# Performance work log

Hardware: AMD Instinct MI355X
Metric: run time of the kernel (lower is better)

Reference implementation:

```python
import jax, jax.numpy as jnp
import numpy as np

N = 100000      # nodes
K = 16          # neighbors per node
C_IN = 16
C1 = 64
C2 = 128
C_OUT = 40


def setup_inputs() -> dict:
    key = jax.random.key(0)
    ks = jax.random.split(key, 12)
    x = jax.random.normal(ks[0], (N, C_IN), dtype=jnp.float32)
    # kNN-style edge list: row = arange(N) repeated K times, col = neighbor ids
    row = jnp.repeat(jnp.arange(N, dtype=jnp.int32), K)
    col = jax.random.randint(ks[1], (N * K,), 0, N, dtype=jnp.int32)
    edge_index = jnp.stack([row, col], axis=0)  # [2, E]
    s = 0.02
    params = {
        'W1': jax.random.normal(ks[2], (2 * C_IN, C1), jnp.float32) * s,
        'b1': jnp.zeros((C1,), jnp.float32),
        'W2': jax.random.normal(ks[3], (C1, C1), jnp.float32) * s,
        'b2': jnp.zeros((C1,), jnp.float32),
        'W3': jax.random.normal(ks[4], (2 * C1, C2), jnp.float32) * s,
        'b3': jnp.zeros((C2,), jnp.float32),
        'W4': jax.random.normal(ks[5], (C2, C2), jnp.float32) * s,
        'b4': jnp.zeros((C2,), jnp.float32),
        'W5': jax.random.normal(ks[6], (C2, C2), jnp.float32) * s,
        'b5': jnp.zeros((C2,), jnp.float32),
        'W6': jax.random.normal(ks[7], (C2, C_OUT), jnp.float32) * s,
        'b6': jnp.zeros((C_OUT,), jnp.float32),
    }
    return {'x': x, 'edge_index': edge_index, **params}


def _edge_conv(x, row, col, Wa, ba, Wb, bb):
    # gather + diff + concat: [E, 2*C]
    xr = x[row]
    e = jnp.concatenate([xr, x[col] - xr], axis=-1)
    h = jax.nn.relu(e @ Wa + ba)
    return jax.nn.relu(h @ Wb + bb)


def reference(x, edge_index, W1, b1, W2, b2, W3, b3, W4, b4, W5, b5, W6, b6):
    row, col = edge_index[0], edge_index[1]
    h1 = _edge_conv(x, row, col, W1, b1, W2, b2)      # [E, 64]
    # as in the source, conv2 indexes the edge-feature tensor with node ids
    h2 = _edge_conv(h1, row, col, W3, b3, W4, b4)     # [E, 128]
    # max over the K neighbors of each node (edges grouped by row node)
    g = h2.reshape(N, K, C2).max(axis=1)              # [N, 128]
    out = jax.nn.relu(g @ W5 + b5) @ W6 + b6          # [N, out]
    return out
```

## Files before the change

kernel.cpp:

```cpp
#include <hip/hip_runtime.h>


#define NN 100000
#define KNB 16
#define EE (NN * KNB)

#define W2F 0
#define W3F 8
#define W4F 40
#define W5F 72
#define W6F 104
#define NFRAG 116

typedef float floatx4 __attribute__((ext_vector_type(4)));
typedef __bf16 bf16x8 __attribute__((ext_vector_type(8)));

static __device__ __forceinline__ unsigned f2bf_rne_u(float f) {
    unsigned u = __float_as_uint(f);
    return (u + 0x7FFFu + ((u >> 16) & 1u)) >> 16;
}
static __device__ __forceinline__ float bfu2f(unsigned h) {
    return __uint_as_float(h << 16);
}

static __device__ __forceinline__ void split_pack2(float a, float b,
                                                   unsigned& hp, unsigned& lp) {
    unsigned ua = __float_as_uint(a), ub = __float_as_uint(b);
    hp = __builtin_amdgcn_perm(ub, ua, 0x07060302u);
    float ra = a - __uint_as_float(ua & 0xFFFF0000u);
    float rb = b - __uint_as_float(ub & 0xFFFF0000u);
    unsigned la = __float_as_uint(ra), lb = __float_as_uint(rb);
    la = la + 0x7FFFu + ((la >> 16) & 1u);
    lb = lb + 0x7FFFu + ((lb >> 16) & 1u);
    lp = __builtin_amdgcn_perm(lb, la, 0x07060302u);
}

static __device__ __forceinline__ void split8(float4 f0, float4 f1,
                                              bf16x8& ah, bf16x8& al) {
    unsigned hd[4], ld[4];
    split_pack2(f0.x, f0.y, hd[0], ld[0]);
    split_pack2(f0.z, f0.w, hd[1], ld[1]);
    split_pack2(f1.x, f1.y, hd[2], ld[2]);
    split_pack2(f1.z, f1.w, hd[3], ld[3]);
    uint4 H = {hd[0], hd[1], hd[2], hd[3]};
    uint4 L = {ld[0], ld[1], ld[2], ld[3]};
    ah = __builtin_bit_cast(bf16x8, H);
    al = __builtin_bit_cast(bf16x8, L);
}

__global__ __launch_bounds__(256) void kw_kernel(
    const float* __restrict__ W2, const float* __restrict__ W3,
    const float* __restrict__ W4, const float* __restrict__ W5,
    const float* __restrict__ W6,
    unsigned short* __restrict__ WH, unsigned short* __restrict__ WL)
{
    int d = blockIdx.x * 256 + threadIdx.x;
    if (d >= NFRAG * 64) return;
    int f = d >> 6, l = d & 63, c = l & 15, q = l >> 4;
    float v[8];
    if (f < W3F) {
        int fx = f - W2F, kc = fx >> 2, nt = fx & 3;
        int k0 = kc * 32 + q * 8, n = nt * 16 + c;
#pragma unroll
        for (int j = 0; j < 8; ++j) v[j] = W2[(k0 + j) * 64 + n];
    } else if (f < W4F) {
        int fx = f - W3F, kc = fx >> 4, nt = fx & 15;
        int k0 = kc * 32 + q * 8, n = nt * 16 + c;
#pragma unroll
        for (int j = 0; j < 8; ++j) {
            int k = k0 + j;
            v[j] = (n < 128) ? (W3[k * 128 + n] - W3[(64 + k) * 128 + n])
                             : W3[(64 + k) * 128 + (n - 128)];
        }
    } else if (f < W5F) {
        int fx = f - W4F, kc = fx >> 3, nt = fx & 7;
        int k0 = kc * 32 + q * 8, n = nt * 16 + c;
#pragma unroll
        for (int j = 0; j < 8; ++j) v[j] = W4[(k0 + j) * 128 + n];
    } else if (f < W6F) {
        int fx = f - W5F, kc = fx >> 3, nt = fx & 7;
        int k0 = kc * 32 + q * 8, n = nt * 16 + c;
#pragma unroll
        for (int j = 0; j < 8; ++j) v[j] = W5[(k0 + j) * 128 + n];
    } else {
        int fx = f - W6F, kc = fx / 3, nt = fx % 3;
        int k0 = kc * 32 + q * 8, n = nt * 16 + c;
#pragma unroll
        for (int j = 0; j < 8; ++j)
            v[j] = (n < 40) ? W6[(k0 + j) * 40 + n] : 0.0f;
    }
    unsigned hs[8], ls[8];
#pragma unroll
    for (int j = 0; j < 8; ++j) {
        unsigned h = f2bf_rne_u(v[j]);
        float r = v[j] - bfu2f(h);
        hs[j] = h;
        ls[j] = f2bf_rne_u(r);
    }
    uint4 H, L;
    H.x = hs[0] | (hs[1] << 16); H.y = hs[2] | (hs[3] << 16);
    H.z = hs[4] | (hs[5] << 16); H.w = hs[6] | (hs[7] << 16);
    L.x = ls[0] | (ls[1] << 16); L.y = ls[2] | (ls[3] << 16);
    L.z = ls[4] | (ls[5] << 16); L.w = ls[6] | (ls[7] << 16);
    *(uint4*)(WH + (size_t)d * 8) = H;
    *(uint4*)(WL + (size_t)d * 8) = L;
}

__global__ __launch_bounds__(256) void k1_kernel(
    const float* __restrict__ x, const float* __restrict__ W1,
    const float* __restrict__ b1, float* __restrict__ A1, float* __restrict__ B1)
{
    int gid = blockIdx.x * 256 + threadIdx.x;
    int n = gid >> 6;
    int j = gid & 63;
    const float* xr = x + n * 16;
    float acc_a = b1[j];
    float acc_b = 0.0f;
#pragma unroll
    for (int k = 0; k < 16; ++k) {
        float xv = xr[k];
        float wt = W1[k * 64 + j];
        float wb = W1[(16 + k) * 64 + j];
        acc_a = fmaf(xv, wt - wb, acc_a);
        acc_b = fmaf(xv, wb, acc_b);
    }
    A1[n * 64 + j] = acc_a;
    B1[n * 64 + j] = acc_b;
}

__global__ __launch_bounds__(256) void k2_kernel(
    const int* __restrict__ col,
    const float* __restrict__ A1, const float* __restrict__ B1,
    const unsigned short* __restrict__ WH, const unsigned short* __restrict__ WL,
    const float* __restrict__ b2, const float* __restrict__ b3,
    float* __restrict__ A3, float* __restrict__ B3)
{
    __shared__ __align__(16) float tF[8 * 512];
    __shared__ __align__(16) float hF[8 * 512];
    const int t = threadIdx.x;
    const int i0 = blockIdx.x * 64;

    {
        const int row = t & 63, part = t >> 6;
        int i = i0 + row;
        int nn = i >> 4;
        int ci = col[i];
        const float* ar = A1 + (size_t)nn * 64 + part * 16;
        const float* br = B1 + (size_t)ci * 64 + part * 16;
        int mt = row >> 4, m = row & 15, kc = part >> 1;
        float* base = tF + (mt * 2 + kc) * 512 + m * 8;
#pragma unroll
        for (int h = 0; h < 2; ++h) {
            int qq = (part & 1) * 2 + h;
            float4 a0 = *(const float4*)(ar + h * 8);
            float4 b0 = *(const float4*)(br + h * 8);
            float4 a1 = *(const float4*)(ar + h * 8 + 4);
            float4 b1v = *(const float4*)(br + h * 8 + 4);
            float4 r0, r1;
            r0.x = fmaxf(a0.x + b0.x, 0.0f); r0.y = fmaxf(a0.y + b0.y, 0.0f);
            r0.z = fmaxf(a0.z + b0.z, 0.0f); r0.w = fmaxf(a0.w + b0.w, 0.0f);
            r1.x = fmaxf(a1.x + b1v.x, 0.0f); r1.y = fmaxf(a1.y + b1v.y, 0.0f);
            r1.z = fmaxf(a1.z + b1v.z, 0.0f); r1.w = fmaxf(a1.w + b1v.w, 0.0f);
            *(float4*)(base + qq * 128) = r0;
            *(float4*)(base + qq * 128 + 4) = r1;
        }
    }
    __syncthreads();

    const int w = __builtin_amdgcn_readfirstlane(t >> 6);
    const int lane = t & 63;

    floatx4 acc1[4];
#pragma unroll
    for (int nt = 0; nt < 4; ++nt) acc1[nt] = (floatx4){0.f, 0.f, 0.f, 0.f};
#pragma unroll
    for (int kc = 0; kc < 2; ++kc) {
        const float* ap = tF + (w * 2 + kc) * 512 + lane * 8;
        bf16x8 ah, al;
        split8(*(const float4*)ap, *(const float4*)(ap + 4), ah, al);
#pragma unroll
        for (int nt = 0; nt < 4; ++nt) {
            size_t fb = (size_t)(W2F + kc * 4 + nt) * 512 + lane * 8;
            bf16x8 bh = __builtin_bit_cast(bf16x8, *(const uint4*)(WH + fb));
            bf16x8 bl = __builtin_bit_cast(bf16x8, *(const uint4*)(WL + fb));
            acc1[nt] = __builtin_amdgcn_mfma_f32_16x16x32_bf16(ah, bh, acc1[nt], 0, 0, 0);
            acc1[nt] = __builtin_amdgcn_mfma_f32_16x16x32_bf16(ah, bl, acc1[nt], 0, 0, 0);
            acc1[nt] = __builtin_amdgcn_mfma_f32_16x16x32_bf16(al, bh, acc1[nt], 0, 0, 0);
        }
    }
    {
        const int qq = lane >> 4, cc = lane & 15;
#pragma unroll
        for (int nt = 0; nt < 4; ++nt) {
            float bv = b2[nt * 16 + cc];
            int colIdx = nt * 16 + cc;
            int kc2 = colIdx >> 5, q2 = (colIdx >> 3) & 3, jj = cc & 7;
            float* dst = hF + (w * 2 + kc2) * 512 + q2 * 128 + jj;
#pragma unroll
            for (int r = 0; r < 4; ++r)
                dst[(qq * 4 + r) * 8] = fmaxf(acc1[nt][r] + bv, 0.0f);
        }
    }
    floatx4 acc2[16];
#pragma unroll
    for (int nt = 0; nt < 16; ++nt) acc2[nt] = (floatx4){0.f, 0.f, 0.f, 0.f};
#pragma unroll
    for (int kc = 0; kc < 2; ++kc) {
        const float* ap = hF + (w * 2 + kc) * 512 + lane * 8;
        bf16x8 ah, al;
        split8(*(const float4*)ap, *(const float4*)(ap + 4), ah, al);
#pragma unroll
        for (int nt = 0; nt < 16; ++nt) {
            size_t fb = (size_t)(W3F + kc * 16 + nt) * 512 + lane * 8;
            bf16x8 bh = __builtin_bit_cast(bf16x8, *(const uint4*)(WH + fb));
            bf16x8 bl = __builtin_bit_cast(bf16x8, *(const uint4*)(WL + fb));
            acc2[nt] = __builtin_amdgcn_mfma_f32_16x16x32_bf16(ah, bh, acc2[nt], 0, 0, 0);
            acc2[nt] = __builtin_amdgcn_mfma_f32_16x16x32_bf16(ah, bl, acc2[nt], 0, 0, 0);
            acc2[nt] = __builtin_amdgcn_mfma_f32_16x16x32_bf16(al, bh, acc2[nt], 0, 0, 0);
        }
    }
    {
        const int qq = lane >> 4, cc = lane & 15;
#pragma unroll
        for (int nt = 0; nt < 16; ++nt) {
            int n = nt * 16 + cc;
            float bv = (n < 128) ? b3[n] : 0.0f;
#pragma unroll
            for (int r = 0; r < 4; ++r) {
                int i = i0 + w * 16 + qq * 4 + r;
                if (i < NN) {
                    float vv = acc2[nt][r];
                    if (n < 128) A3[(size_t)i * 128 + n] = vv + bv;
                    else         B3[(size_t)i * 128 + (n - 128)] = vv;
                }
            }
        }
    }
}

__global__ __launch_bounds__(256) void k3_kernel(
    const int* __restrict__ col,
    const float* __restrict__ A3, const float* __restrict__ B3,
    const unsigned short* __restrict__ WH, const unsigned short* __restrict__ WL,
    const float* __restrict__ b4, float* __restrict__ g)
{
    __shared__ __align__(16) unsigned short aHi[8192];
    __shared__ __align__(16) unsigned short aLo[8192];
    const int t = threadIdx.x;
    const int node0 = blockIdx.x * 4;
    const int e0 = node0 * KNB;
    const int row = t & 63;
    const int kcm = t >> 6;

    {
        const int c = col[e0 + row];
        const int mt = row >> 4, m = row & 15;
        const float* brow = B3 + (size_t)c * 128 + kcm * 32;
        const float* arow = A3 + (size_t)(node0 + mt) * 128 + kcm * 32;
        const int base = (mt * 4 + kcm) * 512 + m * 8;
#pragma unroll
        for (int q = 0; q < 4; ++q) {
            float4 b0 = *(const float4*)(brow + q * 8);
            float4 b1 = *(const float4*)(brow + q * 8 + 4);
            float4 a0 = *(const float4*)(arow + q * 8);
            float4 a1 = *(const float4*)(arow + q * 8 + 4);
            float v0 = fmaxf(a0.x + b0.x, 0.0f), v1 = fmaxf(a0.y + b0.y, 0.0f);
            float v2 = fmaxf(a0.z + b0.z, 0.0f), v3 = fmaxf(a0.w + b0.w, 0.0f);
            float v4 = fmaxf(a1.x + b1.x, 0.0f), v5 = fmaxf(a1.y + b1.y, 0.0f);
            float v6 = fmaxf(a1.z + b1.z, 0.0f), v7 = fmaxf(a1.w + b1.w, 0.0f);
            uint4 H, L;
            split_pack2(v0, v1, H.x, L.x);
            split_pack2(v2, v3, H.y, L.y);
            split_pack2(v4, v5, H.z, L.z);
            split_pack2(v6, v7, H.w, L.w);
            *(uint4*)(aHi + base + q * 128) = H;
            *(uint4*)(aLo + base + q * 128) = L;
        }
    }
    __syncthreads();

    const int wv = t >> 6;
    const int lane = t & 63;
    const int ntb = wv * 2;
    floatx4 acc[4][2];
#pragma unroll
    for (int mt = 0; mt < 4; ++mt)
#pragma unroll
        for (int ntl = 0; ntl < 2; ++ntl)
            acc[mt][ntl] = (floatx4){0.0f, 0.0f, 0.0f, 0.0f};

    for (int kc = 0; kc < 4; ++kc) {
        bf16x8 bh[2], bl[2];
#pragma unroll
        for (int ntl = 0; ntl < 2; ++ntl) {
            int nt = ntb + ntl;
            bh[ntl] = __builtin_bit_cast(bf16x8,
                *(const uint4*)(WH + (size_t)((kc * 8 + nt) * 64 + lane) * 8));
            bl[ntl] = __builtin_bit_cast(bf16x8,
                *(const uint4*)(WL + (size_t)((kc * 8 + nt) * 64 + lane) * 8));
        }
        bf16x8 ah[4], al[4];
#pragma unroll
        for (int mt = 0; mt < 4; ++mt) {
            ah[mt] = __builtin_bit_cast(bf16x8,
                *(const uint4*)(aHi + (mt * 4 + kc) * 512 + lane * 8));
            al[mt] = __builtin_bit_cast(bf16x8,
                *(const uint4*)(aLo + (mt * 4 + kc) * 512 + lane * 8));
        }
#pragma unroll
        for (int mt = 0; mt < 4; ++mt)
#pragma unroll
            for (int ntl = 0; ntl < 2; ++ntl) {
                acc[mt][ntl] = __builtin_amdgcn_mfma_f32_16x16x32_bf16(
                    ah[mt], bh[ntl], acc[mt][ntl], 0, 0, 0);
                acc[mt][ntl] = __builtin_amdgcn_mfma_f32_16x16x32_bf16(
                    ah[mt], bl[ntl], acc[mt][ntl], 0, 0, 0);
                acc[mt][ntl] = __builtin_amdgcn_mfma_f32_16x16x32_bf16(
                    al[mt], bh[ntl], acc[mt][ntl], 0, 0, 0);
            }
    }

#pragma unroll
    for (int mt = 0; mt < 4; ++mt)
#pragma unroll
        for (int ntl = 0; ntl < 2; ++ntl) {
            floatx4 a = acc[mt][ntl];
            float mm = fmaxf(fmaxf(a[0], a[1]), fmaxf(a[2], a[3]));
            mm = fmaxf(mm, __shfl_xor(mm, 16));
            mm = fmaxf(mm, __shfl_xor(mm, 32));
            if (lane < 16) {
                int ccol = (ntb + ntl) * 16 + lane;
                g[(size_t)(node0 + mt) * 128 + ccol] =
                    fmaxf(mm + b4[ccol], 0.0f);
            }
        }
}

__global__ __launch_bounds__(256) void k4_kernel(
    const float* __restrict__ g,
    const unsigned short* __restrict__ WH, const unsigned short* __restrict__ WL,
    const float* __restrict__ b5, const float* __restrict__ b6,
    float* __restrict__ out)
{
    __shared__ __align__(16) float gF[16 * 512];
    const int t = threadIdx.x;
    const int n0 = blockIdx.x * 64;

    {
        const int row = t & 63, part = t >> 6;
        int gn = n0 + row; if (gn >= NN) gn = NN - 1;
        const float* gr = g + (size_t)gn * 128 + part * 32;
        int mt = row >> 4, m = row & 15;
        float* base = gF + (mt * 4 + part) * 512 + m * 8;
#pragma unroll
        for (int qq = 0; qq < 4; ++qq) {
            *(float4*)(base + qq * 128)     = *(const float4*)(gr + qq * 8);
            *(float4*)(base + qq * 128 + 4) = *(const float4*)(gr + qq * 8 + 4);
        }
    }
    __syncthreads();

    const int w = __builtin_amdgcn_readfirstlane(t >> 6);
    const int lane = t & 63;

    floatx4 acc1[8];
#pragma unroll
    for (int nt = 0; nt < 8; ++nt) acc1[nt] = (floatx4){0.f, 0.f, 0.f, 0.f};
#pragma unroll
    for (int kc = 0; kc < 4; ++kc) {
        const float* ap = gF + (w * 4 + kc) * 512 + lane * 8;
        bf16x8 ah, al;
        split8(*(const float4*)ap, *(const float4*)(ap + 4), ah, al);
#pragma unroll
        for (int nt = 0; nt < 8; ++nt) {
            size_t fb = (size_t)(W5F + kc * 8 + nt) * 512 + lane * 8;
            bf16x8 bh = __builtin_bit_cast(bf16x8, *(const uint4*)(WH + fb));
            bf16x8 bl = __builtin_bit_cast(bf16x8, *(const uint4*)(WL + fb));
            acc1[nt] = __builtin_amdgcn_mfma_f32_16x16x32_bf16(ah, bh, acc1[nt], 0, 0, 0);
            acc1[nt] = __builtin_amdgcn_mfma_f32_16x16x32_bf16(ah, bl, acc1[nt], 0, 0, 0);
            acc1[nt] = __builtin_amdgcn_mfma_f32_16x16x32_bf16(al, bh, acc1[nt], 0, 0, 0);
        }
    }
    {
        const int qq = lane >> 4, cc = lane & 15;
#pragma unroll
        for (int nt = 0; nt < 8; ++nt) {
            float bv = b5[nt * 16 + cc];
            int colIdx = nt * 16 + cc;
            int kc2 = colIdx >> 5, q2 = (colIdx >> 3) & 3, jj = cc & 7;
            float* dst = gF + (w * 4 + kc2) * 512 + q2 * 128 + jj;
#pragma unroll
            for (int r = 0; r < 4; ++r)
                dst[(qq * 4 + r) * 8] = fmaxf(acc1[nt][r] + bv, 0.0f);
        }
    }
    floatx4 acc2[3];
#pragma unroll
    for (int nt = 0; nt < 3; ++nt) acc2[nt] = (floatx4){0.f, 0.f, 0.f, 0.f};
#pragma unroll
    for (int kc = 0; kc < 4; ++kc) {
        const float* ap = gF + (w * 4 + kc) * 512 + lane * 8;
        bf16x8 ah, al;
        split8(*(const float4*)ap, *(const float4*)(ap + 4), ah, al);
#pragma unroll
        for (int nt = 0; nt < 3; ++nt) {
            size_t fb = (size_t)(W6F + kc * 3 + nt) * 512 + lane * 8;
            bf16x8 bh = __builtin_bit_cast(bf16x8, *(const uint4*)(WH + fb));
            bf16x8 bl = __builtin_bit_cast(bf16x8, *(const uint4*)(WL + fb));
            acc2[nt] = __builtin_amdgcn_mfma_f32_16x16x32_bf16(ah, bh, acc2[nt], 0, 0, 0);
            acc2[nt] = __builtin_amdgcn_mfma_f32_16x16x32_bf16(ah, bl, acc2[nt], 0, 0, 0);
            acc2[nt] = __builtin_amdgcn_mfma_f32_16x16x32_bf16(al, bh, acc2[nt], 0, 0, 0);
        }
    }
    {
        const int qq = lane >> 4, cc = lane & 15;
#pragma unroll
        for (int nt = 0; nt < 3; ++nt) {
            int n = nt * 16 + cc;
            if (n < 40) {
                float bv = b6[n];
#pragma unroll
                for (int r = 0; r < 4; ++r) {
                    int i = n0 + w * 16 + qq * 4 + r;
                    if (i < NN)
                        out[(size_t)i * 40 + n] = acc2[nt][r] + bv;
                }
            }
        }
    }
}

extern "C" void kernel_launch(void* const* d_in, const int* in_sizes, int n_in,
                              void* d_out, int out_size, void* d_ws, size_t ws_size,
                              hipStream_t stream)
{
    const float* x  = (const float*)d_in[0];
    const int* ei   = (const int*)d_in[1];
    const int* col  = ei + EE;
    const float* W1 = (const float*)d_in[2];
    const float* b1 = (const float*)d_in[3];
    const float* W2 = (const float*)d_in[4];
    const float* b2 = (const float*)d_in[5];
    const float* W3 = (const float*)d_in[6];
    const float* b3 = (const float*)d_in[7];
    const float* W4 = (const float*)d_in[8];
    const float* b4 = (const float*)d_in[9];
    const float* W5 = (const float*)d_in[10];
    const float* b5 = (const float*)d_in[11];
    const float* W6 = (const float*)d_in[12];
    const float* b6 = (const float*)d_in[13];
    float* out = (float*)d_out;

    float* A1 = (float*)d_ws;
    float* B1 = A1 + (size_t)NN * 64;
    float* A3 = B1 + (size_t)NN * 64;
    float* B3 = A3 + (size_t)NN * 128;
    unsigned short* WH = (unsigned short*)(B3 + (size_t)NN * 128);
    unsigned short* WL = WH + NFRAG * 512;
    float* g  = A1;

    kw_kernel<<<(NFRAG * 64 + 255) / 256, 256, 0, stream>>>(W2, W3, W4, W5, W6, WH, WL);
    k1_kernel<<<NN * 64 / 256, 256, 0, stream>>>(x, W1, b1, A1, B1);
    k2_kernel<<<(NN + 63) / 64, 256, 0, stream>>>(col, A1, B1, WH, WL, b2, b3, A3, B3);
    k3_kernel<<<NN / 4, 256, 0, stream>>>(col, A3, B3,
                                          WH + (size_t)W4F * 512, WL + (size_t)W4F * 512,
                                          b4, g);
    k4_kernel<<<(NN + 63) / 64, 256, 0, stream>>>(g, WH, WL, b5, b6, out);
}
```

Baseline: 482.5 us.

## Build k3 MFMA A-fragments in registers, two nodes per wave

The k3 kernel no longer stages the gathered, ReLU'd, bf16-split edge features in shared memory behind a __syncthreads. Each lane now loads its A3/B3 slices directly into the MFMA A-fragment layout, and each wave owns two nodes across all 128 output columns. Blocks cover 8 nodes instead of 4, which halves the grid and lets each weight fragment load feed two nodes. This removes LDS traffic and the block barrier, but raises register pressure (16 accumulators plus 16 A fragments) and each lane now reads 32-byte pieces with strided access.

New measurement: 572.7 us. +18.7%, slower.

```diff
diff --git a/kernel.cpp b/kernel.cpp
--- a/kernel.cpp
+++ b/kernel.cpp
@@ -244,26 +244,25 @@
     const unsigned short* __restrict__ WH, const unsigned short* __restrict__ WL,
     const float* __restrict__ b4, float* __restrict__ g)
 {
-    __shared__ __align__(16) unsigned short aHi[8192];
-    __shared__ __align__(16) unsigned short aLo[8192];
     const int t = threadIdx.x;
-    const int node0 = blockIdx.x * 4;
-    const int e0 = node0 * KNB;
-    const int row = t & 63;
-    const int kcm = t >> 6;
-
-    {
-        const int c = col[e0 + row];
-        const int mt = row >> 4, m = row & 15;
-        const float* brow = B3 + (size_t)c * 128 + kcm * 32;
-        const float* arow = A3 + (size_t)(node0 + mt) * 128 + kcm * 32;
-        const int base = (mt * 4 + kcm) * 512 + m * 8;
-#pragma unroll
-        for (int q = 0; q < 4; ++q) {
-            float4 b0 = *(const float4*)(brow + q * 8);
-            float4 b1 = *(const float4*)(brow + q * 8 + 4);
-            float4 a0 = *(const float4*)(arow + q * 8);
-            float4 a1 = *(const float4*)(arow + q * 8 + 4);
+    const int w = t >> 6;
+    const int lane = t & 63;
+    const int m = lane & 15, q = lane >> 4;
+    const int nodeBase = blockIdx.x * 8 + w * 2;
+
+    bf16x8 aH[2][4], aL[2][4];
+#pragma unroll
+    for (int ng = 0; ng < 2; ++ng) {
+        const int node = nodeBase + ng;
+        const int c = col[node * KNB + m];
+        const float* br = B3 + (size_t)c * 128 + q * 8;
+        const float* ar = A3 + (size_t)node * 128 + q * 8;
+#pragma unroll
+        for (int kc = 0; kc < 4; ++kc) {
+            float4 b0 = *(const float4*)(br + kc * 32);
+            float4 b1 = *(const float4*)(br + kc * 32 + 4);
+            float4 a0 = *(const float4*)(ar + kc * 32);
+            float4 a1 = *(const float4*)(ar + kc * 32 + 4);
             float v0 = fmaxf(a0.x + b0.x, 0.0f), v1 = fmaxf(a0.y + b0.y, 0.0f);
             float v2 = fmaxf(a0.z + b0.z, 0.0f), v3 = fmaxf(a0.w + b0.w, 0.0f);
             float v4 = fmaxf(a1.x + b1.x, 0.0f), v5 = fmaxf(a1.y + b1.y, 0.0f);
@@ -273,67 +272,52 @@
             split_pack2(v2, v3, H.y, L.y);
             split_pack2(v4, v5, H.z, L.z);
             split_pack2(v6, v7, H.w, L.w);
-            *(uint4*)(aHi + base + q * 128) = H;
-            *(uint4*)(aLo + base + q * 128) = L;
-        }
-    }
-    __syncthreads();
-
-    const int wv = t >> 6;
-    const int lane = t & 63;
-    const int ntb = wv * 2;
-    floatx4 acc[4][2];
-#pragma unroll
-    for (int mt = 0; mt < 4; ++mt)
-#pragma unroll
-        for (int ntl = 0; ntl < 2; ++ntl)
-            acc[mt][ntl] = (floatx4){0.0f, 0.0f, 0.0f, 0.0f};
-
+            aH[ng][kc] = __builtin_bit_cast(bf16x8, H);
+            aL[ng][kc] = __builtin_bit_cast(bf16x8, L);
+        }
+    }
+
+    floatx4 acc[2][8];
+#pragma unroll
+    for (int ng = 0; ng < 2; ++ng)
+#pragma unroll
+        for (int nt = 0; nt < 8; ++nt)
+            acc[ng][nt] = (floatx4){0.0f, 0.0f, 0.0f, 0.0f};
+
+#pragma unroll
     for (int kc = 0; kc < 4; ++kc) {
-        bf16x8 bh[2], bl[2];
-#pragma unroll
-        for (int ntl = 0; ntl < 2; ++ntl) {
-            int nt = ntb + ntl;
-            bh[ntl] = __builtin_bit_cast(bf16x8,
-                *(const uint4*)(WH + (size_t)((kc * 8 + nt) * 64 + lane) * 8));
-            bl[ntl] = __builtin_bit_cast(bf16x8,
-                *(const uint4*)(WL + (size_t)((kc * 8 + nt) * 64 + lane) * 8));
-        }
-        bf16x8 ah[4], al[4];
-#pragma unroll
-        for (int mt = 0; mt < 4; ++mt) {
-            ah[mt] = __builtin_bit_cast(bf16x8,
-                *(const uint4*)(aHi + (mt * 4 + kc) * 512 + lane * 8));
-            al[mt] = __builtin_bit_cast(bf16x8,
-                *(const uint4*)(aLo + (mt * 4 + kc) * 512 + lane * 8));
-        }
-#pragma unroll
-        for (int mt = 0; mt < 4; ++mt)
-#pragma unroll
-            for (int ntl = 0; ntl < 2; ++ntl) {
-                acc[mt][ntl] = __builtin_amdgcn_mfma_f32_16x16x32_bf16(
-                    ah[mt], bh[ntl], acc[mt][ntl], 0, 0, 0);
-                acc[mt][ntl] = __builtin_amdgcn_mfma_f32_16x16x32_bf16(
-                    ah[mt], bl[ntl], acc[mt][ntl], 0, 0, 0);
-                acc[mt][ntl] = __builtin_amdgcn_mfma_f32_16x16x32_bf16(
-                    al[mt], bh[ntl], acc[mt][ntl], 0, 0, 0);
+#pragma unroll
+        for (int nt = 0; nt < 8; ++nt) {
+            size_t fb = (size_t)((kc * 8 + nt) * 64 + lane) * 8;
+            bf16x8 bh = __builtin_bit_cast(bf16x8, *(const uint4*)(WH + fb));
+            bf16x8 bl = __builtin_bit_cast(bf16x8, *(const uint4*)(WL + fb));
+#pragma unroll
+            for (int ng = 0; ng < 2; ++ng) {
+                acc[ng][nt] = __builtin_amdgcn_mfma_f32_16x16x32_bf16(
+                    aH[ng][kc], bh, acc[ng][nt], 0, 0, 0);
+                acc[ng][nt] = __builtin_amdgcn_mfma_f32_16x16x32_bf16(
+                    aH[ng][kc], bl, acc[ng][nt], 0, 0, 0);
+                acc[ng][nt] = __builtin_amdgcn_mfma_f32_16x16x32_bf16(
+                    aL[ng][kc], bh, acc[ng][nt], 0, 0, 0);
             }
-    }
-
-#pragma unroll
-    for (int mt = 0; mt < 4; ++mt)
-#pragma unroll
-        for (int ntl = 0; ntl < 2; ++ntl) {
-            floatx4 a = acc[mt][ntl];
+        }
+    }
+
+#pragma unroll
+    for (int ng = 0; ng < 2; ++ng) {
+        const int node = nodeBase + ng;
+#pragma unroll
+        for (int nt = 0; nt < 8; ++nt) {
+            floatx4 a = acc[ng][nt];
             float mm = fmaxf(fmaxf(a[0], a[1]), fmaxf(a[2], a[3]));
             mm = fmaxf(mm, __shfl_xor(mm, 16));
             mm = fmaxf(mm, __shfl_xor(mm, 32));
             if (lane < 16) {
-                int ccol = (ntb + ntl) * 16 + lane;
-                g[(size_t)(node0 + mt) * 128 + ccol] =
-                    fmaxf(mm + b4[ccol], 0.0f);
+                int ccol = nt * 16 + lane;
+                g[(size_t)node * 128 + ccol] = fmaxf(mm + b4[ccol], 0.0f);
             }
         }
+    }
 }
 
 __global__ __launch_bounds__(256) void k4_kernel(
@@ -462,7 +446,7 @@
     kw_kernel<<<(NFRAG * 64 + 255) / 256, 256, 0, stream>>>(W2, W3, W4, W5, W6, WH, WL);
     k1_kernel<<<NN * 64 / 256, 256, 0, stream>>>(x, W1, b1, A1, B1);
     k2_kernel<<<(NN + 63) / 64, 256, 0, stream>>>(col, A1, B1, WH, WL, b2, b3, A3, B3);
-    k3_kernel<<<NN / 4, 256, 0, stream>>>(col, A3, B3,
+    k3_kernel<<<NN / 8, 256, 0, stream>>>(col, A3, B3,
                                           WH + (size_t)W4F * 512, WL + (size_t)W4F * 512,
                                           b4, g);
     k4_kernel<<<(NN + 63) / 64, 256, 0, stream>>>(g, WH, WL, b5, b6, out);
```

## Stage k2 outputs through LDS for coalesced stores and pipeline k3 gathers

Applied to the files above, without the earlier changes.

k2 now writes its MFMA accumulators into a padded shared tile and then stores A3/B3 rows with contiguous float4 writes, replacing the scattered scalar stores. k3 now processes 16 nodes per block in four iterations. It prefetches the next group's B3 neighbor rows into registers while the current group's MFMAs run, and a launch-bounds occupancy hint is added. This is meant to hide gather latency and improve store coalescing, at the cost of extra barriers, more register pressure and fewer blocks in k3.

Result: slower. 637.1 us (+32.0%).

```diff
diff --git a/kernel.cpp b/kernel.cpp
--- a/kernel.cpp
+++ b/kernel.cpp
@@ -135,8 +135,10 @@
     const float* __restrict__ b2, const float* __restrict__ b3,
     float* __restrict__ A3, float* __restrict__ B3)
 {
-    __shared__ __align__(16) float tF[8 * 512];
-    __shared__ __align__(16) float hF[8 * 512];
+    __shared__ __align__(16) float smem[8448];
+    float* tF = smem;
+    float* hF = smem + 4096;
+    float* Tr = smem;
     const int t = threadIdx.x;
     const int i0 = blockIdx.x * 64;
 
@@ -219,26 +221,38 @@
             acc2[nt] = __builtin_amdgcn_mfma_f32_16x16x32_bf16(al, bh, acc2[nt], 0, 0, 0);
         }
     }
+    __syncthreads();
     {
         const int qq = lane >> 4, cc = lane & 15;
 #pragma unroll
-        for (int nt = 0; nt < 16; ++nt) {
-            int n = nt * 16 + cc;
-            float bv = (n < 128) ? b3[n] : 0.0f;
-#pragma unroll
-            for (int r = 0; r < 4; ++r) {
-                int i = i0 + w * 16 + qq * 4 + r;
+        for (int h = 0; h < 2; ++h) {
+#pragma unroll
+            for (int ntl = 0; ntl < 8; ++ntl) {
+                int nt = h * 8 + ntl;
+                int n = ntl * 16 + cc;
+                float bv = (h == 0) ? b3[n] : 0.0f;
+#pragma unroll
+                for (int r = 0; r < 4; ++r)
+                    Tr[(w * 16 + qq * 4 + r) * 132 + n] = acc2[nt][r] + bv;
+            }
+            __syncthreads();
+            {
+                int rowL = t & 63, cg = t >> 6;
+                int i = i0 + rowL;
                 if (i < NN) {
-                    float vv = acc2[nt][r];
-                    if (n < 128) A3[(size_t)i * 128 + n] = vv + bv;
-                    else         B3[(size_t)i * 128 + (n - 128)] = vv;
+                    float* dst = (h == 0 ? A3 : B3) + (size_t)i * 128 + cg * 32;
+                    const float* src = Tr + rowL * 132 + cg * 32;
+#pragma unroll
+                    for (int j = 0; j < 32; j += 4)
+                        *(float4*)(dst + j) = *(const float4*)(src + j);
                 }
             }
-        }
-    }
-}
-
-__global__ __launch_bounds__(256) void k3_kernel(
+            if (h == 0) __syncthreads();
+        }
+    }
+}
+
+__global__ __launch_bounds__(256, 4) void k3_kernel(
     const int* __restrict__ col,
     const float* __restrict__ A3, const float* __restrict__ B3,
     const unsigned short* __restrict__ WH, const unsigned short* __restrict__ WL,
@@ -247,93 +261,115 @@
     __shared__ __align__(16) unsigned short aHi[8192];
     __shared__ __align__(16) unsigned short aLo[8192];
     const int t = threadIdx.x;
-    const int node0 = blockIdx.x * 4;
-    const int e0 = node0 * KNB;
     const int row = t & 63;
     const int kcm = t >> 6;
-
-    {
-        const int c = col[e0 + row];
-        const int mt = row >> 4, m = row & 15;
-        const float* brow = B3 + (size_t)c * 128 + kcm * 32;
-        const float* arow = A3 + (size_t)(node0 + mt) * 128 + kcm * 32;
-        const int base = (mt * 4 + kcm) * 512 + m * 8;
+    const int lane = t & 63;
+    const int wv = t >> 6;
+    const int ntb = wv * 2;
+    const int node00 = blockIdx.x * 16;
+
+    float4 bpre[8];
+    {
+        const int c = col[node00 * KNB + row];
+        const float* br = B3 + (size_t)c * 128 + kcm * 32;
 #pragma unroll
         for (int q = 0; q < 4; ++q) {
-            float4 b0 = *(const float4*)(brow + q * 8);
-            float4 b1 = *(const float4*)(brow + q * 8 + 4);
-            float4 a0 = *(const float4*)(arow + q * 8);
-            float4 a1 = *(const float4*)(arow + q * 8 + 4);
-            float v0 = fmaxf(a0.x + b0.x, 0.0f), v1 = fmaxf(a0.y + b0.y, 0.0f);
-            float v2 = fmaxf(a0.z + b0.z, 0.0f), v3 = fmaxf(a0.w + b0.w, 0.0f);
-            float v4 = fmaxf(a1.x + b1.x, 0.0f), v5 = fmaxf(a1.y + b1.y, 0.0f);
-            float v6 = fmaxf(a1.z + b1.z, 0.0f), v7 = fmaxf(a1.w + b1.w, 0.0f);
-            uint4 H, L;
-            split_pack2(v0, v1, H.x, L.x);
-            split_pack2(v2, v3, H.y, L.y);
-            split_pack2(v4, v5, H.z, L.z);
-            split_pack2(v6, v7, H.w, L.w);
-            *(uint4*)(aHi + base + q * 128) = H;
-            *(uint4*)(aLo + base + q * 128) = L;
-        }
-    }
-    __syncthreads();
-
-    const int wv = t >> 6;
-    const int lane = t & 63;
-    const int ntb = wv * 2;
-    floatx4 acc[4][2];
-#pragma unroll
-    for (int mt = 0; mt < 4; ++mt)
-#pragma unroll
-        for (int ntl = 0; ntl < 2; ++ntl)
-            acc[mt][ntl] = (floatx4){0.0f, 0.0f, 0.0f, 0.0f};
-
-    for (int kc = 0; kc < 4; ++kc) {
-        bf16x8 bh[2], bl[2];
-#pragma unroll
-        for (int ntl = 0; ntl < 2; ++ntl) {
-            int nt = ntb + ntl;
-            bh[ntl] = __builtin_bit_cast(bf16x8,
-                *(const uint4*)(WH + (size_t)((kc * 8 + nt) * 64 + lane) * 8));
-            bl[ntl] = __builtin_bit_cast(bf16x8,
-                *(const uint4*)(WL + (size_t)((kc * 8 + nt) * 64 + lane) * 8));
-        }
-        bf16x8 ah[4], al[4];
-#pragma unroll
-        for (int mt = 0; mt < 4; ++mt) {
-            ah[mt] = __builtin_bit_cast(bf16x8,
-                *(const uint4*)(aHi + (mt * 4 + kc) * 512 + lane * 8));
-            al[mt] = __builtin_bit_cast(bf16x8,
-                *(const uint4*)(aLo + (mt * 4 + kc) * 512 + lane * 8));
-        }
+            bpre[2 * q]     = *(const float4*)(br + q * 8);
+            bpre[2 * q + 1] = *(const float4*)(br + q * 8 + 4);
+        }
+    }
+
+    for (int it = 0; it < 4; ++it) {
+        const int node0 = node00 + it * 4;
+        {
+            const int mt = row >> 4, m = row & 15;
+            const float* ar = A3 + (size_t)(node0 + mt) * 128 + kcm * 32;
+            const int base = (mt * 4 + kcm) * 512 + m * 8;
+#pragma unroll
+            for (int q = 0; q < 4; ++q) {
+                float4 a0 = *(const float4*)(ar + q * 8);
+                float4 a1 = *(const float4*)(ar + q * 8 + 4);
+                float4 b0 = bpre[2 * q], b1 = bpre[2 * q + 1];
+                float v0 = fmaxf(a0.x + b0.x, 0.0f), v1 = fmaxf(a0.y + b0.y, 0.0f);
+                float v2 = fmaxf(a0.z + b0.z, 0.0f), v3 = fmaxf(a0.w + b0.w, 0.0f);
+                float v4 = fmaxf(a1.x + b1.x, 0.0f), v5 = fmaxf(a1.y + b1.y, 0.0f);
+                float v6 = fmaxf(a1.z + b1.z, 0.0f), v7 = fmaxf(a1.w + b1.w, 0.0f);
+                uint4 H, L;
+                split_pack2(v0, v1, H.x, L.x);
+                split_pack2(v2, v3, H.y, L.y);
+                split_pack2(v4, v5, H.z, L.z);
+                split_pack2(v6, v7, H.w, L.w);
+                *(uint4*)(aHi + base + q * 128) = H;
+                *(uint4*)(aLo + base + q * 128) = L;
+            }
+        }
+        __syncthreads();
+
+        if (it < 3) {
+            const int c = col[(node0 + 4) * KNB + row];
+            const float* br = B3 + (size_t)c * 128 + kcm * 32;
+#pragma unroll
+            for (int q = 0; q < 4; ++q) {
+                bpre[2 * q]     = *(const float4*)(br + q * 8);
+                bpre[2 * q + 1] = *(const float4*)(br + q * 8 + 4);
+            }
+        }
+
+        floatx4 acc[4][2];
 #pragma unroll
         for (int mt = 0; mt < 4; ++mt)
 #pragma unroll
+            for (int ntl = 0; ntl < 2; ++ntl)
+                acc[mt][ntl] = (floatx4){0.0f, 0.0f, 0.0f, 0.0f};
+
+#pragma unroll
+        for (int kc = 0; kc < 4; ++kc) {
+            bf16x8 bh[2], bl[2];
+#pragma unroll
             for (int ntl = 0; ntl < 2; ++ntl) {
-                acc[mt][ntl] = __builtin_amdgcn_mfma_f32_16x16x32_bf16(
-                    ah[mt], bh[ntl], acc[mt][ntl], 0, 0, 0);
-                acc[mt][ntl] = __builtin_amdgcn_mfma_f32_16x16x32_bf16(
-                    ah[mt], bl[ntl], acc[mt][ntl], 0, 0, 0);
-                acc[mt][ntl] = __builtin_amdgcn_mfma_f32_16x16x32_bf16(
-                    al[mt], bh[ntl], acc[mt][ntl], 0, 0, 0);
-            }
-    }
-
-#pragma unroll
-    for (int mt = 0; mt < 4; ++mt)
-#pragma unroll
-        for (int ntl = 0; ntl < 2; ++ntl) {
-            floatx4 a = acc[mt][ntl];
-            float mm = fmaxf(fmaxf(a[0], a[1]), fmaxf(a[2], a[3]));
-            mm = fmaxf(mm, __shfl_xor(mm, 16));
-            mm = fmaxf(mm, __shfl_xor(mm, 32));
-            if (lane < 16) {
-                int ccol = (ntb + ntl) * 16 + lane;
-                g[(size_t)(node0 + mt) * 128 + ccol] =
-                    fmaxf(mm + b4[ccol], 0.0f);
-            }
-        }
+                int nt = ntb + ntl;
+                bh[ntl] = __builtin_bit_cast(bf16x8,
+                    *(const uint4*)(WH + (size_t)((kc * 8 + nt) * 64 + lane) * 8));
+                bl[ntl] = __builtin_bit_cast(bf16x8,
+                    *(const uint4*)(WL + (size_t)((kc * 8 + nt) * 64 + lane) * 8));
+            }
+            bf16x8 ah[4], al[4];
+#pragma unroll
+            for (int mt = 0; mt < 4; ++mt) {
+                ah[mt] = __builtin_bit_cast(bf16x8,
+                    *(const uint4*)(aHi + (mt * 4 + kc) * 512 + lane * 8));
+                al[mt] = __builtin_bit_cast(bf16x8,
+                    *(const uint4*)(aLo + (mt * 4 + kc) * 512 + lane * 8));
+            }
+#pragma unroll
+            for (int mt = 0; mt < 4; ++mt)
+#pragma unroll
+                for (int ntl = 0; ntl < 2; ++ntl) {
+                    acc[mt][ntl] = __builtin_amdgcn_mfma_f32_16x16x32_bf16(
+                        ah[mt], bh[ntl], acc[mt][ntl], 0, 0, 0);
+                    acc[mt][ntl] = __builtin_amdgcn_mfma_f32_16x16x32_bf16(
+                        ah[mt], bl[ntl], acc[mt][ntl], 0, 0, 0);
+                    acc[mt][ntl] = __builtin_amdgcn_mfma_f32_16x16x32_bf16(
+                        al[mt], bh[ntl], acc[mt][ntl], 0, 0, 0);
+                }
+        }
+
+#pragma unroll
+        for (int mt = 0; mt < 4; ++mt)
+#pragma unroll
+            for (int ntl = 0; ntl < 2; ++ntl) {
+                floatx4 a = acc[mt][ntl];
+                float mm = fmaxf(fmaxf(a[0], a[1]), fmaxf(a[2], a[3]));
+                mm = fmaxf(mm, __shfl_xor(mm, 16));
+                mm = fmaxf(mm, __shfl_xor(mm, 32));
+                if (lane < 16) {
+                    int ccol = (ntb + ntl) * 16 + lane;
+                    g[(size_t)(node0 + mt) * 128 + ccol] =
+                        fmaxf(mm + b4[ccol], 0.0f);
+                }
+            }
+        __syncthreads();
+    }
 }
 
 __global__ __launch_bounds__(256) void k4_kernel(
@@ -462,8 +498,8 @@
     kw_kernel<<<(NFRAG * 64 + 255) / 256, 256, 0, stream>>>(W2, W3, W4, W5, W6, WH, WL);
     k1_kernel<<<NN * 64 / 256, 256, 0, stream>>>(x, W1, b1, A1, B1);
     k2_kernel<<<(NN + 63) / 64, 256, 0, stream>>>(col, A1, B1, WH, WL, b2, b3, A3, B3);
-    k3_kernel<<<NN / 4, 256, 0, stream>>>(col, A3, B3,
-                                          WH + (size_t)W4F * 512, WL + (size_t)W4F * 512,
-                                          b4, g);
+    k3_kernel<<<NN / 16, 256, 0, stream>>>(col, A3, B3,
+                                           WH + (size_t)W4F * 512, WL + (size_t)W4F * 512,
+                                           b4, g);
     k4_kernel<<<(NN + 63) / 64, 256, 0, stream>>>(g, WH, WL, b5, b6, out);
 }
```
